# Kernel optimization log

Measured on AMD Instinct MI355X. Metric: run time of the kernel, lower is better.

The kernel has to match this reference:

```python
import jax, jax.numpy as jnp
import numpy as np

N_HEADS = 16
N_KV_HEADS = 4
HEAD_DIM = 128
ROPE_BASE = 10000.0


def _rms_norm(x):
    eps = jnp.asarray(jnp.finfo(x.dtype).eps, x.dtype)
    return x * jax.lax.rsqrt(jnp.mean(x * x, axis=-1, keepdims=True) + eps)


def _rope_tables(T, dtype):
    d = HEAD_DIM
    inv_freq = 1.0 / (ROPE_BASE ** (jnp.arange(0, d, 2, dtype=jnp.float32) / d))
    freqs = jnp.outer(jnp.arange(T, dtype=jnp.float32), inv_freq)  # [T, d/2]
    return jnp.cos(freqs).astype(dtype), jnp.sin(freqs).astype(dtype)


def _apply_rope(x, cos, sin):
    # x: [B, H, T, D]; cos/sin: [T, D/2]
    d = x.shape[-1] // 2
    x1, x2 = x[..., :d], x[..., d:]
    return jnp.concatenate((x1 * cos + x2 * sin, -x1 * sin + x2 * cos), axis=-1)


def setup_inputs() -> dict:
    key = jax.random.key(0)
    ks = jax.random.split(key, 5)
    B, T, C = 2, 2048, 2048
    kv_dim = N_KV_HEADS * HEAD_DIM
    s = 0.02
    return {
        "x": jax.random.normal(ks[0], (B, T, C), jnp.float32),
        "Wq": jax.random.normal(ks[1], (C, C), jnp.float32) * s,
        "Wk": jax.random.normal(ks[2], (kv_dim, C), jnp.float32) * s,
        "Wv": jax.random.normal(ks[3], (kv_dim, C), jnp.float32) * s,
        "Wo": jax.random.normal(ks[4], (C, C), jnp.float32) * s,
    }


def reference(x, Wq, Wk, Wv, Wo):
    B, T, C = x.shape
    g = N_HEADS // N_KV_HEADS

    # QKV projections (torch Linear: x @ W.T), split into heads -> [B, H, T, D]
    q = (x @ Wq.T).reshape(B, T, N_HEADS, HEAD_DIM).transpose(0, 2, 1, 3)
    k = (x @ Wk.T).reshape(B, T, N_KV_HEADS, HEAD_DIM).transpose(0, 2, 1, 3)
    v = (x @ Wv.T).reshape(B, T, N_KV_HEADS, HEAD_DIM).transpose(0, 2, 1, 3)

    # QK RMSNorm (no learned weight)
    q, k = _rms_norm(q), _rms_norm(k)

    # RoPE
    cos, sin = _rope_tables(T, q.dtype)
    q, k = _apply_rope(q, cos, sin), _apply_rope(k, cos, sin)

    # GQA: expand kv heads
    k = jnp.repeat(k, g, axis=1)
    v = jnp.repeat(v, g, axis=1)

    # causal SDPA
    scale = 1.0 / jnp.sqrt(jnp.asarray(HEAD_DIM, q.dtype))
    scores = jnp.einsum("bhqd,bhkd->bhqk", q, k) * scale
    mask = jnp.tril(jnp.ones((T, T), bool))
    scores = jnp.where(mask, scores, jnp.asarray(-jnp.inf, scores.dtype))
    att = jax.nn.softmax(scores, axis=-1)
    y = jnp.einsum("bhqk,bhkd->bhqd", att, v)

    y = y.transpose(0, 2, 1, 3).reshape(B, T, C)
    return y @ Wo.T
```

## Files before the change

### kernel.cpp

```cpp
#include <hip/hip_runtime.h>
#include <hip/hip_bf16.h>
#include <cstdint>
#include <math.h>

#define DEVINL __device__ __forceinline__

typedef __attribute__((ext_vector_type(8))) __bf16 bf16x8;
typedef __attribute__((ext_vector_type(4))) float floatx4;
typedef __attribute__((ext_vector_type(4))) int intx4;

constexpr int TB = 2;
constexpr int TT = 2048;
constexpr int TC = 2048;
constexpr int NH = 16, NKV = 4, HD = 128;
constexpr int MR = TB * TT;
constexpr int NQ = NH * HD;
constexpr int NK = NKV * HD;
constexpr int NQKV = NQ + 2 * NK;

DEVINL unsigned bfbits(float f) {
  unsigned u = __builtin_bit_cast(unsigned, f);
  return (u + 0x7FFFu + ((u >> 16) & 1u)) >> 16;
}
DEVINL int pk2(float a, float b) {
  union { __hip_bfloat162 h; int i; } u;
  u.h = __float22bfloat162_rn(float2{a, b});
  return u.i;
}
DEVINL void gl_lds16(const __hip_bfloat16* g, __hip_bfloat16* l) {
  __builtin_amdgcn_global_load_lds(
      (const __attribute__((address_space(1))) unsigned int*)g,
      (__attribute__((address_space(3))) unsigned int*)l, 16, 0, 0);
}
DEVINL floatx4 mfma16(bf16x8 a, bf16x8 b, floatx4 c) {
  return __builtin_amdgcn_mfma_f32_16x16x32_bf16(a, b, c, 0, 0, 0);
}
DEVINL void cstore(float* p, float v) { *p = v; }
DEVINL void cstore(__hip_bfloat16* p, float v) { *(unsigned short*)p = (unsigned short)bfbits(v); }

__global__ __launch_bounds__(256) void k_cvt5(
    const float* __restrict__ s0, const float* __restrict__ s1,
    const float* __restrict__ s2, const float* __restrict__ s3,
    const float* __restrict__ s4,
    __hip_bfloat16* __restrict__ d0, __hip_bfloat16* __restrict__ d1,
    __hip_bfloat16* __restrict__ d2, __hip_bfloat16* __restrict__ d3,
    __hip_bfloat16* __restrict__ d4) {
  const float* s;
  __hip_bfloat16* d;
  int n;
  switch (blockIdx.y) {
    case 0: s = s0; d = d0; n = MR * TC; break;
    case 1: s = s1; d = d1; n = NQ * TC; break;
    case 2: s = s2; d = d2; n = NK * TC; break;
    case 3: s = s3; d = d3; n = NK * TC; break;
    default: s = s4; d = d4; n = TC * TC; break;
  }
  int i = (blockIdx.x * 256 + threadIdx.x) * 4;
  if (i >= n) return;
  float4 v = *(const float4*)(s + i);
  ushort4 o;
  o.x = (unsigned short)bfbits(v.x);
  o.y = (unsigned short)bfbits(v.y);
  o.z = (unsigned short)bfbits(v.z);
  o.w = (unsigned short)bfbits(v.w);
  *(ushort4*)(d + i) = o;
}

template <typename OUT_T>
__global__ __launch_bounds__(256, 2) void k_gemm_bt(
    const __hip_bfloat16* __restrict__ A, const __hip_bfloat16* __restrict__ B,
    OUT_T* __restrict__ C, int M, int N, int K) {
  __shared__ __align__(16) __hip_bfloat16 As[128 * 64];
  __shared__ __align__(16) __hip_bfloat16 Bs[128 * 64];
  const int tid = threadIdx.x;
  const int lane = tid & 63, w = tid >> 6;
  const int q15 = lane & 15, quad = lane >> 4;
  const int wm = w >> 1, wn = w & 1;
  const int tm = blockIdx.y, tn = blockIdx.x;

  const int r0 = tid >> 3;
  const int csw = ((tid & 7) ^ (r0 & 7)) * 8;
  const __hip_bfloat16* ag = A + (size_t)(tm * 128 + r0) * K + csw;
  const __hip_bfloat16* bg = B + (size_t)(tn * 128 + r0) * K + csw;
  __hip_bfloat16* lA = As + (tid & ~63) * 8;
  __hip_bfloat16* lB = Bs + (tid & ~63) * 8;

  floatx4 acc[4][4] = {};
  for (int k0 = 0; k0 < K; k0 += 64) {
    __syncthreads();
#pragma unroll
    for (int i = 0; i < 4; i++) {
      gl_lds16(ag + (size_t)(i * 32) * K + k0, lA + i * 2048);
      gl_lds16(bg + (size_t)(i * 32) * K + k0, lB + i * 2048);
    }
    __syncthreads();
#pragma unroll
    for (int kh = 0; kh < 2; kh++) {
      bf16x8 af[4], bfr[4];
#pragma unroll
      for (int i = 0; i < 4; i++)
        af[i] = *(const bf16x8*)(As + (wm * 64 + i * 16 + q15) * 64 +
                                 (((kh * 4 + quad) ^ (q15 & 7)) * 8));
#pragma unroll
      for (int i = 0; i < 4; i++)
        bfr[i] = *(const bf16x8*)(Bs + (wn * 64 + i * 16 + q15) * 64 +
                                  (((kh * 4 + quad) ^ (q15 & 7)) * 8));
#pragma unroll
      for (int mi = 0; mi < 4; mi++)
#pragma unroll
        for (int ni = 0; ni < 4; ni++)
          acc[mi][ni] = mfma16(af[mi], bfr[ni], acc[mi][ni]);
    }
  }
#pragma unroll
  for (int mi = 0; mi < 4; mi++) {
    int row0 = tm * 128 + wm * 64 + mi * 16 + quad * 4;
#pragma unroll
    for (int ni = 0; ni < 4; ni++) {
      int col = tn * 128 + wn * 64 + ni * 16 + q15;
#pragma unroll
      for (int r = 0; r < 4; r++)
        cstore(C + (size_t)(row0 + r) * N + col, acc[mi][ni][r]);
    }
  }
}

__global__ __launch_bounds__(256, 2) void k_gemm_qkv(
    const __hip_bfloat16* __restrict__ A, const __hip_bfloat16* __restrict__ B,
    __hip_bfloat16* __restrict__ q_l, __hip_bfloat16* __restrict__ k_l,
    __hip_bfloat16* __restrict__ vt) {
  constexpr int K = TC;
  __shared__ __align__(16) __hip_bfloat16 smem[128 * 130];
  __hip_bfloat16* As = smem;
  __hip_bfloat16* Bs = smem + 128 * 64;
  const int tid = threadIdx.x;
  const int lane = tid & 63, w = tid >> 6;
  const int q15 = lane & 15, quad = lane >> 4;
  const int wm = w >> 1, wn = w & 1;
  const int tm = blockIdx.y, tn = blockIdx.x;

  const int r0 = tid >> 3;
  const int csw = ((tid & 7) ^ (r0 & 7)) * 8;
  const __hip_bfloat16* ag = A + (size_t)(tm * 128 + r0) * K + csw;
  const __hip_bfloat16* bg = B + (size_t)(tn * 128 + r0) * K + csw;
  __hip_bfloat16* lA = As + (tid & ~63) * 8;
  __hip_bfloat16* lB = Bs + (tid & ~63) * 8;

  floatx4 acc[4][4] = {};
  for (int k0 = 0; k0 < K; k0 += 64) {
    __syncthreads();
#pragma unroll
    for (int i = 0; i < 4; i++) {
      gl_lds16(ag + (size_t)(i * 32) * K + k0, lA + i * 2048);
      gl_lds16(bg + (size_t)(i * 32) * K + k0, lB + i * 2048);
    }
    __syncthreads();
#pragma unroll
    for (int kh = 0; kh < 2; kh++) {
      bf16x8 af[4], bfr[4];
#pragma unroll
      for (int i = 0; i < 4; i++)
        af[i] = *(const bf16x8*)(As + (wm * 64 + i * 16 + q15) * 64 +
                                 (((kh * 4 + quad) ^ (q15 & 7)) * 8));
#pragma unroll
      for (int i = 0; i < 4; i++)
        bfr[i] = *(const bf16x8*)(Bs + (wn * 64 + i * 16 + q15) * 64 +
                                  (((kh * 4 + quad) ^ (q15 & 7)) * 8));
#pragma unroll
      for (int mi = 0; mi < 4; mi++)
#pragma unroll
        for (int ni = 0; ni < 4; ni++)
          acc[mi][ni] = mfma16(af[mi], bfr[ni], acc[mi][ni]);
    }
  }

  __syncthreads();
#pragma unroll
  for (int mi = 0; mi < 4; mi++)
#pragma unroll
    for (int ni = 0; ni < 4; ni++) {
      int row = wm * 64 + mi * 16 + quad * 4;
      int col = wn * 64 + ni * 16 + q15;
#pragma unroll
      for (int r = 0; r < 4; r++)
        *(unsigned short*)(smem + (row + r) * 130 + col) =
            (unsigned short)bfbits(acc[mi][ni][r]);
    }
  __syncthreads();

  const int b = tm >> 4;
  if (tn < NH + NKV) {
    const bool isq = tn < NH;
    const int h = isq ? tn : tn - NH;
    const float scale = isq ? (1.4426950408889634f * 0.08838834764831845f) : 1.0f;
    __hip_bfloat16* base = isq ? q_l + (size_t)(b * NH + h) * TT * HD
                               : k_l + (size_t)(b * NKV + h) * TT * HD;
    const float ifreq = exp2f((float)lane * -(13.287712379549449f / 64.0f));
    for (int j = 0; j < 32; ++j) {
      int row = w * 32 + j;
      int t = (tm & 15) * 128 + row;
      float x1 = __bfloat162float(smem[row * 130 + lane]);
      float x2 = __bfloat162float(smem[row * 130 + 64 + lane]);
      float ss = x1 * x1 + x2 * x2;
#pragma unroll
      for (int m = 1; m < 64; m <<= 1) ss += __shfl_xor(ss, m, 64);
      float rinv = rsqrtf(ss * (1.0f / 128.0f) + 1.1920928955078125e-07f);
      float ang = (float)t * ifreq;
      float sv = sinf(ang), cv = cosf(ang);
      float o1 = (x1 * cv + x2 * sv) * rinv * scale;
      float o2 = (x2 * cv - x1 * sv) * rinv * scale;
      __hip_bfloat16* dst = base + (size_t)t * HD;
      *(unsigned short*)(dst + lane) = (unsigned short)bfbits(o1);
      *(unsigned short*)(dst + lane + 64) = (unsigned short)bfbits(o2);
    }
  } else {
    const int hv = tn - NH - NKV;
    __hip_bfloat16* vbase = vt + (size_t)(b * NKV + hv) * HD * TT + (tm & 15) * 128;
    for (int j = 0; j < 64; ++j) {
      int e = j * 256 + tid;
      int d = e >> 7, tt = e & 127;
      vbase[(size_t)d * TT + tt] = smem[tt * 130 + d];
    }
  }
}

__global__ __launch_bounds__(256, 2) void k_attn(
    const __hip_bfloat16* __restrict__ q_l, const __hip_bfloat16* __restrict__ k_l,
    const __hip_bfloat16* __restrict__ vt_l, __hip_bfloat16* __restrict__ y) {
  __shared__ __align__(16) __hip_bfloat16 Ks[2][64 * 128];
  __shared__ __align__(16) __hip_bfloat16 Vs[2][128 * 64];
  const int tid = threadIdx.x, lane = tid & 63, w = tid >> 6;
  const int q15 = lane & 15, quad = lane >> 4;
  const int id = blockIdx.x;
  const int sl = id >> 5;
  const int qt = (sl < 8) ? (15 - sl) : (sl - 8);
  const int h = id & 15, b = (id >> 4) & 1;
  const int hk = h >> 2;
  const int nkb = 2 * qt + 2;

  const __hip_bfloat16* kbase = k_l + (size_t)(b * NKV + hk) * TT * HD;
  const __hip_bfloat16* vbase = vt_l + (size_t)(b * NKV + hk) * HD * TT;
  const __hip_bfloat16* qbase = q_l + ((size_t)(b * NH + h) * TT + qt * 128) * HD;

  auto stage = [&](int kb, int buf) {
#pragma unroll
    for (int i = 0; i < 4; i++) {
      int s = i * 256 + tid;
      int rk = s >> 4, ck = s & 15;
      gl_lds16(kbase + (size_t)(kb * 64 + rk) * HD + (ck ^ (rk & 15)) * 8,
               Ks[buf] + (i * 256 + (tid & ~63)) * 8);
      int rv = s >> 3, cv = s & 7;
      gl_lds16(vbase + (size_t)rv * TT + kb * 64 + (cv ^ (rv & 7)) * 8,
               Vs[buf] + (i * 256 + (tid & ~63)) * 8);
    }
  };

  bf16x8 qf[4][2];
#pragma unroll
  for (int dc = 0; dc < 4; dc++)
#pragma unroll
    for (int qh = 0; qh < 2; qh++)
      qf[dc][qh] = *(const bf16x8*)(qbase + (size_t)(w * 32 + qh * 16 + q15) * HD +
                                    dc * 32 + quad * 8);

  floatx4 ot[8][2] = {};
  float lsum[2] = {0.0f, 0.0f};
  int cur = 0;
  const int kb_last_w = 2 * qt + (w >> 1);

  for (int kb = 0; kb < nkb; kb++) {
    __syncthreads();
    if (kb == 0) {
      stage(0, cur);
      __syncthreads();
    }
    if (kb + 1 < nkb) stage(kb + 1, cur ^ 1);

    if (kb <= kb_last_w) {
      floatx4 st[4][2] = {};
#pragma unroll
      for (int kt = 0; kt < 4; kt++) {
        int r = kt * 16 + q15;
#pragma unroll
        for (int dc = 0; dc < 4; dc++) {
          int c = dc * 4 + quad;
          bf16x8 kf = *(const bf16x8*)(Ks[cur] + (r * 16 + (c ^ (r & 15))) * 8);
          st[kt][0] = mfma16(kf, qf[dc][0], st[kt][0]);
          st[kt][1] = mfma16(kf, qf[dc][1], st[kt][1]);
        }
      }
      if (kb >= 2 * qt) {
#pragma unroll
        for (int qh = 0; qh < 2; qh++) {
          int qg = qt * 128 + w * 32 + qh * 16 + q15;
#pragma unroll
          for (int kt = 0; kt < 4; kt++)
#pragma unroll
            for (int r = 0; r < 4; r++)
              if (kb * 64 + kt * 16 + quad * 4 + r > qg) st[kt][qh][r] = -INFINITY;
        }
      }
      int pA[2][4], pB[2][4];
#pragma unroll
      for (int kt = 0; kt < 4; kt++) {
#pragma unroll
        for (int qh = 0; qh < 2; qh++) {
          float p0 = exp2f(st[kt][qh][0]);
          float p1 = exp2f(st[kt][qh][1]);
          float p2 = exp2f(st[kt][qh][2]);
          float p3 = exp2f(st[kt][qh][3]);
          lsum[qh] += (p0 + p1) + (p2 + p3);
          pA[qh][kt] = pk2(p0, p1);
          pB[qh][kt] = pk2(p2, p3);
        }
      }
#pragma unroll
      for (int kc = 0; kc < 2; kc++) {
        bf16x8 pf[2];
#pragma unroll
        for (int qh = 0; qh < 2; qh++) {
          int u0 = pA[qh][2 * kc], u1 = pA[qh][2 * kc + 1];
          int v0 = pB[qh][2 * kc], v1 = pB[qh][2 * kc + 1];
          asm("v_permlane32_swap_b32 %0, %1" : "+v"(u0), "+v"(u1));
          asm("v_permlane16_swap_b32 %0, %1" : "+v"(u0), "+v"(u1));
          asm("v_permlane32_swap_b32 %0, %1" : "+v"(v0), "+v"(v1));
          asm("v_permlane16_swap_b32 %0, %1" : "+v"(v0), "+v"(v1));
          intx4 wi;
          wi[0] = u0; wi[1] = v0; wi[2] = u1; wi[3] = v1;
          pf[qh] = __builtin_bit_cast(bf16x8, wi);
        }
#pragma unroll
        for (int dt = 0; dt < 8; dt++) {
          int r = dt * 16 + q15, c = kc * 4 + quad;
          bf16x8 vf = *(const bf16x8*)(Vs[cur] + (r * 8 + (c ^ (r & 7))) * 8);
          ot[dt][0] = mfma16(vf, pf[0], ot[dt][0]);
          ot[dt][1] = mfma16(vf, pf[1], ot[dt][1]);
        }
      }
    }
    cur ^= 1;
  }
#pragma unroll
  for (int qh = 0; qh < 2; qh++) {
    float ls = lsum[qh];
    ls += __shfl_xor(ls, 16, 64);
    ls += __shfl_xor(ls, 32, 64);
    float linv = 1.0f / ls;
    int t = qt * 128 + w * 32 + qh * 16 + q15;
    __hip_bfloat16* yrow = y + (size_t)(b * TT + t) * TC + h * HD;
#pragma unroll
    for (int dt = 0; dt < 8; dt++) {
      int d = dt * 16 + quad * 4;
      ushort4 o;
      o.x = (unsigned short)bfbits(ot[dt][qh][0] * linv);
      o.y = (unsigned short)bfbits(ot[dt][qh][1] * linv);
      o.z = (unsigned short)bfbits(ot[dt][qh][2] * linv);
      o.w = (unsigned short)bfbits(ot[dt][qh][3] * linv);
      *(ushort4*)(yrow + d) = o;
    }
  }
}

extern "C" void kernel_launch(void* const* d_in, const int* in_sizes, int n_in,
                              void* d_out, int out_size, void* d_ws, size_t ws_size,
                              hipStream_t stream) {
  (void)in_sizes; (void)n_in; (void)out_size; (void)ws_size;
  const float* x  = (const float*)d_in[0];
  const float* Wq = (const float*)d_in[1];
  const float* Wk = (const float*)d_in[2];
  const float* Wv = (const float*)d_in[3];
  const float* Wo = (const float*)d_in[4];
  float* out = (float*)d_out;

  char* ws = (char*)d_ws;
  size_t off = 0;
  auto alloc = [&](size_t bytes) {
    void* p = ws + off;
    off += (bytes + 255) & ~(size_t)255;
    return p;
  };
  __hip_bfloat16* xb   = (__hip_bfloat16*)alloc((size_t)MR * TC * 2);
  __hip_bfloat16* wqkv = (__hip_bfloat16*)alloc((size_t)NQKV * TC * 2);
  __hip_bfloat16* wo   = (__hip_bfloat16*)alloc((size_t)TC * TC * 2);
  __hip_bfloat16* q_l  = (__hip_bfloat16*)alloc((size_t)TB * NH * TT * HD * 2);
  __hip_bfloat16* k_l  = (__hip_bfloat16*)alloc((size_t)TB * NKV * TT * HD * 2);
  __hip_bfloat16* vt_l = (__hip_bfloat16*)alloc((size_t)TB * NKV * HD * TT * 2);
  __hip_bfloat16* yb   = (__hip_bfloat16*)alloc((size_t)MR * TC * 2);

  k_cvt5<<<dim3((MR * TC / 4 + 255) / 256, 5), 256, 0, stream>>>(
      x, Wq, Wk, Wv, Wo,
      xb, wqkv, wqkv + (size_t)NQ * TC, wqkv + (size_t)(NQ + NK) * TC, wo);

  k_gemm_qkv<<<dim3(NQKV / 128, MR / 128), 256, 0, stream>>>(
      xb, wqkv, q_l, k_l, vt_l);

  k_attn<<<(TT / 128) * NH * TB, 256, 0, stream>>>(q_l, k_l, vt_l, yb);

  k_gemm_bt<float><<<dim3(TC / 128, MR / 128), 256, 0, stream>>>(
      yb, wo, out, MR, TC, TC);
}
```

Measured before the change: 290.6 us.

## Flatten cvt grid, use rotation recurrence for RoPE, vectorize V transpose stores

The conversion kernel now uses a flat 1D grid partitioned by cumulative segment sizes, which removes the many idle blocks the old 2D grid launched for the smaller weight matrices. The RoPE epilogue replaces per-row sinf/cosf with an angle-addition recurrence seeded once per warp, which trades some accuracy drift over 32 steps for cheaper math. The V transpose writes 8 bf16 values as one 16-byte store instead of scalar 2-byte stores, so global writes are coalesced.

```diff
diff --git a/kernel.cpp b/kernel.cpp
--- a/kernel.cpp
+++ b/kernel.cpp
@@ -38,6 +38,11 @@
 DEVINL void cstore(float* p, float v) { *p = v; }
 DEVINL void cstore(__hip_bfloat16* p, float v) { *(unsigned short*)p = (unsigned short)bfbits(v); }
 
+constexpr int C0 = MR * TC / 4;
+constexpr int C1 = C0 + NQ * TC / 4;
+constexpr int C2 = C1 + NK * TC / 4;
+constexpr int C3 = C2 + NK * TC / 4;
+constexpr int C4 = C3 + TC * TC / 4;
 __global__ __launch_bounds__(256) void k_cvt5(
     const float* __restrict__ s0, const float* __restrict__ s1,
     const float* __restrict__ s2, const float* __restrict__ s3,
@@ -45,18 +50,18 @@
     __hip_bfloat16* __restrict__ d0, __hip_bfloat16* __restrict__ d1,
     __hip_bfloat16* __restrict__ d2, __hip_bfloat16* __restrict__ d3,
     __hip_bfloat16* __restrict__ d4) {
+  int gid = blockIdx.x * 256 + threadIdx.x;
   const float* s;
   __hip_bfloat16* d;
-  int n;
-  switch (blockIdx.y) {
-    case 0: s = s0; d = d0; n = MR * TC; break;
-    case 1: s = s1; d = d1; n = NQ * TC; break;
-    case 2: s = s2; d = d2; n = NK * TC; break;
-    case 3: s = s3; d = d3; n = NK * TC; break;
-    default: s = s4; d = d4; n = TC * TC; break;
-  }
-  int i = (blockIdx.x * 256 + threadIdx.x) * 4;
-  if (i >= n) return;
+  int base;
+  if (gid < C1) {
+    if (gid < C0) { s = s0; d = d0; base = 0; }
+    else          { s = s1; d = d1; base = C0; }
+  } else if (gid < C3) {
+    if (gid < C2) { s = s2; d = d2; base = C1; }
+    else          { s = s3; d = d3; base = C2; }
+  } else            { s = s4; d = d4; base = C3; }
+  int i = (gid - base) * 4;
   float4 v = *(const float4*)(s + i);
   ushort4 o;
   o.x = (unsigned short)bfbits(v.x);
@@ -196,30 +201,39 @@
     __hip_bfloat16* base = isq ? q_l + (size_t)(b * NH + h) * TT * HD
                                : k_l + (size_t)(b * NKV + h) * TT * HD;
     const float ifreq = exp2f((float)lane * -(13.287712379549449f / 64.0f));
+    const int t0 = (tm & 15) * 128 + w * 32;
+    float cv = cosf((float)t0 * ifreq), sv = sinf((float)t0 * ifreq);
+    const float cF = cosf(ifreq), sF = sinf(ifreq);
     for (int j = 0; j < 32; ++j) {
       int row = w * 32 + j;
-      int t = (tm & 15) * 128 + row;
+      int t = t0 + j;
       float x1 = __bfloat162float(smem[row * 130 + lane]);
       float x2 = __bfloat162float(smem[row * 130 + 64 + lane]);
       float ss = x1 * x1 + x2 * x2;
 #pragma unroll
       for (int m = 1; m < 64; m <<= 1) ss += __shfl_xor(ss, m, 64);
       float rinv = rsqrtf(ss * (1.0f / 128.0f) + 1.1920928955078125e-07f);
-      float ang = (float)t * ifreq;
-      float sv = sinf(ang), cv = cosf(ang);
       float o1 = (x1 * cv + x2 * sv) * rinv * scale;
       float o2 = (x2 * cv - x1 * sv) * rinv * scale;
       __hip_bfloat16* dst = base + (size_t)t * HD;
       *(unsigned short*)(dst + lane) = (unsigned short)bfbits(o1);
       *(unsigned short*)(dst + lane + 64) = (unsigned short)bfbits(o2);
+      float cn = cv * cF - sv * sF;
+      sv = sv * cF + cv * sF;
+      cv = cn;
     }
   } else {
     const int hv = tn - NH - NKV;
     __hip_bfloat16* vbase = vt + (size_t)(b * NKV + hv) * HD * TT + (tm & 15) * 128;
-    for (int j = 0; j < 64; ++j) {
+#pragma unroll
+    for (int j = 0; j < 8; ++j) {
       int e = j * 256 + tid;
-      int d = e >> 7, tt = e & 127;
-      vbase[(size_t)d * TT + tt] = smem[tt * 130 + d];
+      int d = e >> 4, tt0 = (e & 15) * 8;
+      union { unsigned short u[8]; uint4 q; } pk;
+#pragma unroll
+      for (int i = 0; i < 8; ++i)
+        pk.u[i] = *(const unsigned short*)(smem + (tt0 + i) * 130 + d);
+      *(uint4*)(vbase + (size_t)d * TT + tt0) = pk.q;
     }
   }
 }
@@ -387,7 +401,7 @@
   __hip_bfloat16* vt_l = (__hip_bfloat16*)alloc((size_t)TB * NKV * HD * TT * 2);
   __hip_bfloat16* yb   = (__hip_bfloat16*)alloc((size_t)MR * TC * 2);
 
-  k_cvt5<<<dim3((MR * TC / 4 + 255) / 256, 5), 256, 0, stream>>>(
+  k_cvt5<<<C4 / 256, 256, 0, stream>>>(
       x, Wq, Wk, Wv, Wo,
       xb, wqkv, wqkv + (size_t)NQ * TC, wqkv + (size_t)(NQ + NK) * TC, wo);
 
```

New measurement: 290.4 us (median of 2 runs). About the same (-0.1%).
